# Kernel tuning notes

Hardware: AMD Instinct MI355X
Metric: run time of the kernel (lower is better)

Reference implementation:

```python
import jax, jax.numpy as jnp
import numpy as np

B, N, C = 8, 8192, 256
H = 8            # num_heads
D = C // H       # head dim = 32
P = 64           # proj_size (Linformer rank)


def setup_inputs() -> dict:
    key = jax.random.key(0)
    ks = jax.random.split(key, 12)
    s = lambda fan_in: 1.0 / np.sqrt(fan_in)
    return {
        "x": jax.random.normal(ks[0], (B, N, C), jnp.float32),
        "Wqkvv": jax.random.normal(ks[1], (4 * C, C), jnp.float32) * s(C),
        "WE": jax.random.normal(ks[2], (P, N), jnp.float32) * s(N),
        "bE": jax.random.normal(ks[3], (P,), jnp.float32) * s(N),
        "WF": jax.random.normal(ks[4], (P, N), jnp.float32) * s(N),
        "bF": jax.random.normal(ks[5], (P,), jnp.float32) * s(N),
        "Wo1": jax.random.normal(ks[6], (C // 2, C), jnp.float32) * s(C),
        "bo1": jax.random.normal(ks[7], (C // 2,), jnp.float32) * s(C),
        "Wo2": jax.random.normal(ks[8], (C // 2, C), jnp.float32) * s(C),
        "bo2": jax.random.normal(ks[9], (C // 2,), jnp.float32) * s(C),
        "temp1": jnp.ones((H, 1, 1), jnp.float32),
        "temp2": jnp.ones((H, 1, 1), jnp.float32),
    }


def _l2norm(v, axis=-1, eps=1e-12):
    # matches torch F.normalize
    n = jnp.sqrt(jnp.sum(v * v, axis=axis, keepdims=True))
    return v / jnp.maximum(n, eps)


def reference(x, Wqkvv, WE, bE, WF, bF, Wo1, bo1, Wo2, bo2, temp1, temp2):
    b, n, c = x.shape
    # qkvv: [b,n,4c] -> [4,b,h,d,n]  (includes the .transpose(-2,-1) of each part)
    qkvv = jnp.einsum('bnc,fc->bnf', x, Wqkvv).reshape(b, n, 4, H, D)
    qkvv = qkvv.transpose(2, 0, 3, 4, 1)
    q, k, v_ca, v_sa = qkvv[0], qkvv[1], qkvv[2], qkvv[3]  # each [b,h,d,n]

    # Linformer-style low-rank projections along the token axis
    k_proj = jnp.einsum('bhdn,pn->bhdp', k, WE) + bE   # [b,h,d,p]
    v_proj = jnp.einsum('bhdn,pn->bhdp', v_sa, WF) + bF

    qn = _l2norm(q)
    kn = _l2norm(k)

    # --- channel attention branch (XCiT-style) ---
    attn_ca = jnp.einsum('bhdn,bhen->bhde', qn, kn) * temp1[None]  # [b,h,d,d]
    attn_ca = jax.nn.softmax(attn_ca, axis=-1)  # dropout: eval mode (identity)
    x_ca = jnp.einsum('bhde,bhen->bhdn', attn_ca, v_ca)
    x_ca = x_ca.transpose(0, 3, 1, 2).reshape(b, n, c)  # [b,n,c]

    # --- spatial attention branch (low-rank) ---
    attn_sa = jnp.einsum('bhdn,bhdp->bhnp', qn, k_proj) * temp2[None]  # [b,h,n,p]
    attn_sa = jax.nn.softmax(attn_sa, axis=-1)
    x_sa = jnp.einsum('bhnp,bhdp->bhnd', attn_sa, v_proj)  # [b,h,n,d]
    # faithful to original: permute(0,3,1,2).reshape(b,n,c)
    x_sa = x_sa.transpose(0, 3, 1, 2).reshape(b, n, c)

    x_sa = jnp.einsum('bnc,oc->bno', x_sa, Wo1) + bo1
    x_ca = jnp.einsum('bnc,oc->bno', x_ca, Wo2) + bo2
    return jnp.concatenate((x_sa, x_ca), axis=-1)
```

## Files before the change

kernel.cpp:

```cpp
#include <hip/hip_runtime.h>
#include <hip/hip_bf16.h>
#include <stdint.h>


typedef __attribute__((ext_vector_type(8))) __bf16 bf16x8;
typedef __attribute__((ext_vector_type(4))) __bf16 bf16x4;
typedef __attribute__((ext_vector_type(4))) float f32x4;

#define MFMA(a, b, c) __builtin_amdgcn_mfma_f32_16x16x32_bf16((a), (b), (c), 0, 0, 0)

__device__ __forceinline__ void gl2lds16(const __bf16* g, __bf16* l) {
  __builtin_amdgcn_global_load_lds(
      (const __attribute__((address_space(1))) void*)(const void*)g,
      (__attribute__((address_space(3))) void*)(void*)l, 16, 0, 0);
}

__device__ __forceinline__ int detect_f32(const unsigned int* __restrict__ xw) {
  int c = 0;
#pragma unroll
  for (int i = 0; i < 64; ++i) {
    const unsigned int u = xw[i];
    c += (((u >> 7) & 0xFF) >= 0xC0) ? 1 : 0;
    c += (((u >> 23) & 0xFF) >= 0xC0) ? 1 : 0;
  }
  return c > 8;
}

__global__ __launch_bounds__(256) void k_convert_x(const void* __restrict__ src,
                                                   __bf16* __restrict__ dst) {
  const int i = (blockIdx.x * 256 + threadIdx.x) * 8;
  if (detect_f32((const unsigned int*)src)) {
    const float* s = (const float*)src;
    bf16x8 v;
#pragma unroll
    for (int j = 0; j < 8; ++j) v[j] = (__bf16)s[i + j];
    *(bf16x8*)(dst + i) = v;
  } else {
    *(bf16x8*)(dst + i) = *(const bf16x8*)((const __bf16*)src + i);
  }
}

__global__ __launch_bounds__(256) void k_convert_w(
    const void* s0, const void* s1, const void* s2, const void* s3, const void* s4,
    const void* s5, const void* s6, const void* s7, const void* s8, const void* s9,
    const void* s10, __bf16* __restrict__ cw, const void* __restrict__ xsrc) {
  const int i = (blockIdx.x * 256 + threadIdx.x) * 8;
  if (i >= 1376656) return;
  const void* s;
  int base;
  if (i < 262144)        { s = s0;  base = 0; }
  else if (i < 786432)   { s = s1;  base = 262144; }
  else if (i < 786496)   { s = s2;  base = 786432; }
  else if (i < 1310784)  { s = s3;  base = 786496; }
  else if (i < 1310848)  { s = s4;  base = 1310784; }
  else if (i < 1343616)  { s = s5;  base = 1310848; }
  else if (i < 1343744)  { s = s6;  base = 1343616; }
  else if (i < 1376512)  { s = s7;  base = 1343744; }
  else if (i < 1376640)  { s = s8;  base = 1376512; }
  else if (i < 1376648)  { s = s9;  base = 1376640; }
  else                   { s = s10; base = 1376648; }
  const int li = i - base;
  if (detect_f32((const unsigned int*)xsrc)) {
    const float* sf = (const float*)s;
#pragma unroll
    for (int j = 0; j < 8; ++j) cw[i + j] = (__bf16)sf[li + j];
  } else {
    const __bf16* sb = (const __bf16*)s;
#pragma unroll
    for (int j = 0; j < 8; ++j) cw[i + j] = sb[li + j];
  }
}

union alignas(16) QkvvSmem {
  struct { __bf16 A[2][4096]; __bf16 B[2][4096]; } k;
  __bf16 C[32 * 136];
};

__global__ __launch_bounds__(256, 5) void k_qkvv(const __bf16* __restrict__ x,
                                                 const __bf16* __restrict__ Wq,
                                                 __bf16* __restrict__ qkvv,
                                                 float* __restrict__ npart) {
  __shared__ QkvvSmem sm;
  const int t = threadIdx.x, lane = t & 63;
  const int wr = t >> 7, wc = (t >> 6) & 1;
  const int l15 = lane & 15, g = lane >> 4;
  const int f0 = blockIdx.y * 128;
  const int t0 = blockIdx.x * 128;
  f32x4 acc[4][4] = {};
  const int r = t >> 2;
  const int c8 = ((t & 3) ^ ((t >> 3) & 3)) * 8;
  const int cx = ((g ^ ((l15 >> 1) & 3)) * 8);
#pragma unroll
  for (int i = 0; i < 2; ++i) {
    gl2lds16(Wq + (size_t)(f0 + i * 64 + r) * 256 + c8, &sm.k.A[0][i * 2048 + t * 8]);
    gl2lds16(x + (size_t)(t0 + i * 64 + r) * 256 + c8, &sm.k.B[0][i * 2048 + t * 8]);
  }
  __syncthreads();
  for (int ks = 0; ks < 8; ++ks) {
    const int cur = ks & 1, nxt = cur ^ 1;
    if (ks < 7) {
      const int k1 = (ks + 1) * 32;
#pragma unroll
      for (int i = 0; i < 2; ++i) {
        gl2lds16(Wq + (size_t)(f0 + i * 64 + r) * 256 + k1 + c8, &sm.k.A[nxt][i * 2048 + t * 8]);
        gl2lds16(x + (size_t)(t0 + i * 64 + r) * 256 + k1 + c8, &sm.k.B[nxt][i * 2048 + t * 8]);
      }
    }
    bf16x8 af[4], bfr[4];
#pragma unroll
    for (int i = 0; i < 4; ++i) {
      af[i] = *(const bf16x8*)(&sm.k.A[cur][(wr * 64 + i * 16 + l15) * 32 + cx]);
      bfr[i] = *(const bf16x8*)(&sm.k.B[cur][(wc * 64 + i * 16 + l15) * 32 + cx]);
    }
#pragma unroll
    for (int i = 0; i < 4; ++i)
#pragma unroll
      for (int j = 0; j < 4; ++j) acc[i][j] = MFMA(af[i], bfr[j], acc[i][j]);
    __syncthreads();
  }
  const int b = t0 >> 13;
  const int n0 = t0 & 8191;
  for (int i = 0; i < 4; ++i) {
    if (i) __syncthreads();
#pragma unroll
    for (int j = 0; j < 4; ++j)
#pragma unroll
      for (int rr = 0; rr < 4; ++rr)
        sm.C[(wr * 16 + g * 4 + rr) * 136 + wc * 64 + j * 16 + l15] = (__bf16)acc[i][j][rr];
    __syncthreads();
#pragma unroll
    for (int half = 0; half < 2; ++half) {
      const int row_l = (t >> 4) + half * 16;
      const int col8 = (t & 15) * 8;
      const bf16x8 v = *(const bf16x8*)(sm.C + row_l * 136 + col8);
      const int f = f0 + (row_l >> 4) * 64 + i * 16 + (row_l & 15);
      *(bf16x8*)(qkvv + (size_t)(((f >> 8) * 8 + b) * 256 + (f & 255)) * 8192 + n0 + col8) = v;
      if (f0 < 512) {
        float s = 0.f;
#pragma unroll
        for (int jj = 0; jj < 8; ++jj) { const float q = (float)v[jj]; s += q * q; }
#pragma unroll
        for (int off = 1; off < 16; off <<= 1) s += __shfl_xor(s, off, 16);
        if ((t & 15) == 0) npart[(size_t)blockIdx.x * 512 + f] = s;
      }
    }
  }
}

__global__ __launch_bounds__(256) void k_nred(const float* __restrict__ npart,
                                              float* __restrict__ qsum,
                                              float* __restrict__ ksum) {
  const int which = blockIdx.x >> 3, b = blockIdx.x & 7;
  const int c = threadIdx.x;
  float s = 0.f;
#pragma unroll 4
  for (int j = 0; j < 64; ++j)
    s += npart[(size_t)(b * 64 + j) * 512 + which * 256 + c];
  (which ? ksum : qsum)[b * 256 + c] = s;
}

__global__ __launch_bounds__(256) void k_proj_part(const __bf16* __restrict__ qkvv,
                                                   const __bf16* __restrict__ WE,
                                                   const __bf16* __restrict__ WF,
                                                   float* __restrict__ pbuf) {
  __shared__ alignas(16) __bf16 As[2][128 * 32];
  __shared__ alignas(16) __bf16 Bs[2][64 * 32];
  const int t = threadIdx.x, lane = t & 63;
  const int wr = t >> 7, wc = (t >> 6) & 1;
  const int l15 = lane & 15, g = lane >> 4;
  const int kc = blockIdx.x, mt = blockIdx.y, pj = blockIdx.z;
  const __bf16* A = qkvv + (size_t)(pj ? 3 : 1) * 2048 * 8192;
  const __bf16* Bm = pj ? WF : WE;
  const int r0 = mt * 128;
  f32x4 acc[4][2] = {};
  const int r = t >> 2;
  const int c8 = ((t & 3) ^ ((t >> 3) & 3)) * 8;
  const int cx = ((g ^ ((l15 >> 1) & 3)) * 8);
  const int kb = kc * 512;
#pragma unroll
  for (int i = 0; i < 2; ++i)
    gl2lds16(A + (size_t)(r0 + i * 64 + r) * 8192 + kb + c8, &As[0][i * 2048 + t * 8]);
  gl2lds16(Bm + (size_t)r * 8192 + kb + c8, &Bs[0][t * 8]);
  __syncthreads();
  for (int ks = 0; ks < 16; ++ks) {
    const int cur = ks & 1, nxt = cur ^ 1;
    if (ks < 15) {
      const int k1 = kb + (ks + 1) * 32;
#pragma unroll
      for (int i = 0; i < 2; ++i)
        gl2lds16(A + (size_t)(r0 + i * 64 + r) * 8192 + k1 + c8, &As[nxt][i * 2048 + t * 8]);
      gl2lds16(Bm + (size_t)r * 8192 + k1 + c8, &Bs[nxt][t * 8]);
    }
    bf16x8 af[4], bfr[2];
#pragma unroll
    for (int i = 0; i < 4; ++i)
      af[i] = *(const bf16x8*)(&As[cur][(wr * 64 + i * 16 + l15) * 32 + cx]);
#pragma unroll
    for (int j = 0; j < 2; ++j)
      bfr[j] = *(const bf16x8*)(&Bs[cur][(wc * 32 + j * 16 + l15) * 32 + cx]);
#pragma unroll
    for (int i = 0; i < 4; ++i)
#pragma unroll
      for (int j = 0; j < 2; ++j) acc[i][j] = MFMA(af[i], bfr[j], acc[i][j]);
    __syncthreads();
  }
  float* dst = pbuf + (size_t)((pj * 16 + kc) * 2048 + r0) * 64;
#pragma unroll
  for (int i = 0; i < 4; ++i)
#pragma unroll
    for (int j = 0; j < 2; ++j)
#pragma unroll
      for (int rr = 0; rr < 4; ++rr)
        dst[(wr * 64 + i * 16 + g * 4 + rr) * 64 + wc * 32 + j * 16 + l15] = acc[i][j][rr];
}

__global__ __launch_bounds__(256) void k_proj_reduce(const float* __restrict__ pbuf,
                                                     const __bf16* __restrict__ bE,
                                                     const __bf16* __restrict__ bF,
                                                     const float* __restrict__ qsum,
                                                     const __bf16* __restrict__ t2,
                                                     __bf16* __restrict__ kprojT,
                                                     __bf16* __restrict__ vprojb) {
  const int idx = blockIdx.x * 256 + threadIdx.x;
  const int pj = idx >> 17, rp = idx & 131071, p = idx & 63;
  const int row = rp >> 6, bh = row >> 5, d = row & 31, h = bh & 7;
  float s = (float)((pj ? bF : bE)[p]);
  const float* src = pbuf + (size_t)pj * 16 * 131072 + rp;
#pragma unroll
  for (int k = 0; k < 16; ++k) s += src[(size_t)k * 131072];
  if (pj == 0) {
    const float qi = 1.0f / fmaxf(sqrtf(qsum[row]), 1e-12f);
    kprojT[bh * 2048 + p * 32 + d] = (__bf16)(s * qi * (float)t2[h]);
  } else {
    vprojb[bh * 2048 + d * 64 + p] = (__bf16)s;
  }
}

__global__ __launch_bounds__(256) void k_sca_part(const __bf16* __restrict__ qkvv,
                                                  float* __restrict__ spart) {
  const int bh = blockIdx.x, kc = blockIdx.y;
  const int t = threadIdx.x, lane = t & 63, w = t >> 6;
  const __bf16* qb = qkvv + (size_t)(bh * 32) * 8192;
  const __bf16* kb = qkvv + (size_t)(2048 + bh * 32) * 8192;
  f32x4 acc[2][2] = {};
  const int kbase = kc * 1024 + w * 256 + (lane >> 4) * 8;
#pragma unroll
  for (int ks = 0; ks < 256; ks += 32) {
    bf16x8 af[2], bfr[2];
#pragma unroll
    for (int i = 0; i < 2; ++i) {
      af[i] = *(const bf16x8*)(qb + (size_t)(i * 16 + (lane & 15)) * 8192 + kbase + ks);
      bfr[i] = *(const bf16x8*)(kb + (size_t)(i * 16 + (lane & 15)) * 8192 + kbase + ks);
    }
#pragma unroll
    for (int i = 0; i < 2; ++i)
#pragma unroll
      for (int j = 0; j < 2; ++j) acc[i][j] = MFMA(af[i], bfr[j], acc[i][j]);
  }
  float* dst = spart + (size_t)((bh * 8 + kc) * 4 + w) * 1024;
#pragma unroll
  for (int i = 0; i < 2; ++i)
#pragma unroll
    for (int j = 0; j < 2; ++j)
#pragma unroll
      for (int rr = 0; rr < 4; ++rr)
        dst[(i * 16 + (lane >> 4) * 4 + rr) * 32 + j * 16 + (lane & 15)] = acc[i][j][rr];
}

__global__ __launch_bounds__(256) void k_sca_softmax(const float* __restrict__ spart,
                                                     const float* __restrict__ qsum,
                                                     const float* __restrict__ ksum,
                                                     const __bf16* __restrict__ temp1,
                                                     __bf16* __restrict__ attnb) {
  const int bh = blockIdx.x;
  __shared__ float S[1024];
  const int t = threadIdx.x;
  const float tmp = (float)temp1[bh & 7];
  for (int idx = t; idx < 1024; idx += 256) {
    float s = 0.f;
    const float* src = spart + (size_t)bh * 32768 + idx;
#pragma unroll
    for (int k = 0; k < 32; ++k) s += src[k * 1024];
    const float qi = 1.0f / fmaxf(sqrtf(qsum[bh * 32 + (idx >> 5)]), 1e-12f);
    const float ki = 1.0f / fmaxf(sqrtf(ksum[bh * 32 + (idx & 31)]), 1e-12f);
    S[idx] = s * qi * ki * tmp;
  }
  __syncthreads();
  const int lane = t & 63, w = t >> 6;
#pragma unroll
  for (int rr = 0; rr < 4; ++rr) {
    const int row = rr * 8 + w * 2 + (lane >> 5);
    const int e = lane & 31;
    float v = S[row * 32 + e];
    float m = v;
#pragma unroll
    for (int off = 16; off; off >>= 1) m = fmaxf(m, __shfl_xor(m, off, 32));
    const float ex = __expf(v - m);
    float sm = ex;
#pragma unroll
    for (int off = 16; off; off >>= 1) sm += __shfl_xor(sm, off, 32);
    attnb[(size_t)bh * 1024 + row * 32 + e] = (__bf16)(ex / sm);
  }
}

union alignas(16) CasaSmem {
  struct { __bf16 V[32 * 264]; __bf16 L[64 * 72]; } ca;
  struct { __bf16 Q[32 * 264]; __bf16 P[4][16 * 72]; __bf16 L[32 * 72]; } sa;
};

__global__ __launch_bounds__(256) void k_casa(const __bf16* __restrict__ qkvv,
                                              const __bf16* __restrict__ attnb,
                                              const __bf16* __restrict__ kprojT,
                                              const __bf16* __restrict__ vprojb,
                                              __bf16* __restrict__ xca,
                                              __bf16* __restrict__ xsa) {
  __shared__ CasaSmem sm;
  const int t = threadIdx.x, lane = t & 63, w = t >> 6;
  const int l15 = lane & 15, g = lane >> 4;
  if (blockIdx.y < 64) {
    const int bh = blockIdx.y, b = bh >> 3, h = bh & 7;
    const __bf16* vb = qkvv + (size_t)(4096 + bh * 32) * 8192;
    {
      const int er = t >> 5, nc8 = (t & 31) * 8;
#pragma unroll
      for (int l = 0; l < 4; ++l) {
        const int e = l * 8 + er;
        *(bf16x8*)(&sm.ca.V[e * 264 + nc8]) =
            *(const bf16x8*)(vb + (size_t)e * 8192 + blockIdx.x * 256 + nc8);
      }
    }
    bf16x8 aa[2];
#pragma unroll
    for (int mi = 0; mi < 2; ++mi)
      aa[mi] = *(const bf16x8*)(attnb + bh * 1024 + (mi * 16 + l15) * 32 + g * 8);
    __syncthreads();
#pragma unroll
    for (int it = 0; it < 4; ++it) {
      const int nl = it * 64 + w * 16 + l15;
      union { bf16x8 v; unsigned short u[8]; } bq;
#pragma unroll
      for (int j = 0; j < 8; ++j)
        bq.u[j] = *(const unsigned short*)(&sm.ca.V[(g * 8 + j) * 264 + nl]);
      f32x4 o[2] = {};
#pragma unroll
      for (int mi = 0; mi < 2; ++mi) o[mi] = MFMA(aa[mi], bq.v, o[mi]);
      if (it) __syncthreads();
#pragma unroll
      for (int mi = 0; mi < 2; ++mi) {
        bf16x4 p4;
#pragma unroll
        for (int rr = 0; rr < 4; ++rr) p4[rr] = (__bf16)o[mi][rr];
        *(bf16x4*)(&sm.ca.L[(w * 16 + l15) * 72 + mi * 16 + g * 4]) = p4;
      }
      __syncthreads();
      {
        const int row = t >> 2, ch = t & 3;
        const bf16x8 v = *(const bf16x8*)(&sm.ca.L[row * 72 + ch * 8]);
        *(bf16x8*)(xca + (size_t)(b * 8192 + blockIdx.x * 256 + it * 64 + row) * 256 +
                   h * 32 + ch * 8) = v;
      }
    }
  } else {
    const int bh = blockIdx.y - 64;
    const __bf16* qb = qkvv + (size_t)(bh * 32) * 8192;
    {
      const int er = t >> 5, nc8 = (t & 31) * 8;
#pragma unroll
      for (int l = 0; l < 4; ++l) {
        const int e = l * 8 + er;
        *(bf16x8*)(&sm.sa.Q[e * 264 + nc8]) =
            *(const bf16x8*)(qb + (size_t)e * 8192 + blockIdx.x * 256 + nc8);
      }
    }
    bf16x8 ka[4], va[2][2];
#pragma unroll
    for (int tile = 0; tile < 4; ++tile)
      ka[tile] = *(const bf16x8*)(kprojT + bh * 2048 + (tile * 16 + l15) * 32 + g * 8);
#pragma unroll
    for (int mi = 0; mi < 2; ++mi)
#pragma unroll
      for (int kh = 0; kh < 2; ++kh)
        va[mi][kh] = *(const bf16x8*)(vprojb + bh * 2048 + (mi * 16 + l15) * 64 + kh * 32 + g * 8);
    __syncthreads();
    __bf16* Pw = &sm.sa.P[w][0];
#pragma unroll
    for (int it = 0; it < 4; ++it) {
      const int nl = it * 64 + w * 16 + l15;
      union { bf16x8 v; unsigned short u[8]; } bq;
#pragma unroll
      for (int j = 0; j < 8; ++j)
        bq.u[j] = *(const unsigned short*)(&sm.sa.Q[(g * 8 + j) * 264 + nl]);
      f32x4 st[4];
#pragma unroll
      for (int tile = 0; tile < 4; ++tile) {
        f32x4 z = {};
        st[tile] = MFMA(ka[tile], bq.v, z);
      }
      float m = st[0][0];
#pragma unroll
      for (int tile = 0; tile < 4; ++tile)
#pragma unroll
        for (int rr = 0; rr < 4; ++rr) m = fmaxf(m, st[tile][rr]);
      m = fmaxf(m, __shfl_xor(m, 16, 64));
      m = fmaxf(m, __shfl_xor(m, 32, 64));
      float sum = 0.f;
#pragma unroll
      for (int tile = 0; tile < 4; ++tile) {
        bf16x4 p4;
#pragma unroll
        for (int rr = 0; rr < 4; ++rr) {
          const float ex = __expf(st[tile][rr] - m);
          sum += ex;
          p4[rr] = (__bf16)ex;
        }
        *(bf16x4*)(Pw + l15 * 72 + tile * 16 + g * 4) = p4;
      }
      sum += __shfl_xor(sum, 16, 64);
      sum += __shfl_xor(sum, 32, 64);
      const float inv = 1.0f / sum;
      f32x4 o[2] = {};
#pragma unroll
      for (int kh = 0; kh < 2; ++kh) {
        const bf16x8 pf = *(const bf16x8*)(Pw + l15 * 72 + kh * 32 + g * 8);
#pragma unroll
        for (int mi = 0; mi < 2; ++mi) o[mi] = MFMA(va[mi][kh], pf, o[mi]);
      }
      if (it) __syncthreads();
#pragma unroll
      for (int mi = 0; mi < 2; ++mi)
#pragma unroll
        for (int rr = 0; rr < 4; ++rr) {
          const int d = mi * 16 + g * 4 + rr;
          sm.sa.L[d * 72 + w * 16 + l15] = (__bf16)(o[mi][rr] * inv);
        }
      __syncthreads();
      {
        const int row = t >> 3, ch = t & 7;
        const bf16x8 v = *(const bf16x8*)(&sm.sa.L[row * 72 + ch * 8]);
        *(bf16x8*)(xsa + (size_t)(bh * 32 + row) * 8192 + blockIdx.x * 256 + it * 64 +
                   ch * 8) = v;
      }
    }
  }
}

__global__ __launch_bounds__(256) void k_out(const __bf16* __restrict__ xsa,
                                             const __bf16* __restrict__ xca,
                                             const __bf16* __restrict__ Wo1,
                                             const __bf16* __restrict__ bo1,
                                             const __bf16* __restrict__ Wo2,
                                             const __bf16* __restrict__ bo2,
                                             void* __restrict__ outv,
                                             const void* __restrict__ xsrc) {
  __shared__ alignas(16) __bf16 As[2][128 * 32];
  __shared__ alignas(16) __bf16 Bs[2][128 * 32];
  const int t = threadIdx.x, lane = t & 63;
  const int wr = t >> 7, wc = (t >> 6) & 1;
  const int l15 = lane & 15, g = lane >> 4;
  const int nt = blockIdx.x, b = blockIdx.y, br = blockIdx.z;
  const int isf32 = detect_f32((const unsigned int*)xsrc);
  const __bf16* Wo = br ? Wo2 : Wo1;
  const __bf16* bo = br ? bo2 : bo1;
  f32x4 acc[4][4] = {};
  const int r = t >> 2;
  const int c8 = ((t & 3) ^ ((t >> 3) & 3)) * 8;
  const int cx = ((g ^ ((l15 >> 1) & 3)) * 8);
  const int row_b = nt * 128 + r;
  auto asrc = [&](int i, int k0) -> const __bf16* {
    const int row = row_b + i * 64;
    if (br == 0)
      return xsa + (size_t)((b * 8 + ((row >> 5) & 7)) * 32 + (row >> 8)) * 8192 +
             (row & 31) * 256 + k0 + c8;
    return xca + (size_t)(b * 8192 + row) * 256 + k0 + c8;
  };
#pragma unroll
  for (int i = 0; i < 2; ++i) {
    gl2lds16(asrc(i, 0), &As[0][i * 2048 + t * 8]);
    gl2lds16(Wo + (size_t)(i * 64 + r) * 256 + c8, &Bs[0][i * 2048 + t * 8]);
  }
  __syncthreads();
  for (int ks = 0; ks < 8; ++ks) {
    const int cur = ks & 1, nxt = cur ^ 1;
    if (ks < 7) {
      const int k1 = (ks + 1) * 32;
#pragma unroll
      for (int i = 0; i < 2; ++i) {
        gl2lds16(asrc(i, k1), &As[nxt][i * 2048 + t * 8]);
        gl2lds16(Wo + (size_t)(i * 64 + r) * 256 + k1 + c8, &Bs[nxt][i * 2048 + t * 8]);
      }
    }
    bf16x8 af[4], bfr[4];
#pragma unroll
    for (int i = 0; i < 4; ++i) {
      af[i] = *(const bf16x8*)(&As[cur][(wr * 64 + i * 16 + l15) * 32 + cx]);
      bfr[i] = *(const bf16x8*)(&Bs[cur][(wc * 64 + i * 16 + l15) * 32 + cx]);
    }
#pragma unroll
    for (int i = 0; i < 4; ++i)
#pragma unroll
      for (int j = 0; j < 4; ++j) acc[i][j] = MFMA(af[i], bfr[j], acc[i][j]);
    __syncthreads();
  }
  float bias[4];
#pragma unroll
  for (int j = 0; j < 4; ++j) bias[j] = (float)bo[wc * 64 + j * 16 + l15];
#pragma unroll
  for (int i = 0; i < 4; ++i) {
#pragma unroll
    for (int j = 0; j < 4; ++j) {
      const int col = wc * 64 + j * 16 + l15;
#pragma unroll
      for (int rr = 0; rr < 4; ++rr) {
        const int row = nt * 128 + wr * 64 + i * 16 + g * 4 + rr;
        const float val = acc[i][j][rr] + bias[j];
        const size_t oi = (size_t)(b * 8192 + row) * 256 + br * 128 + col;
        if (isf32) ((float*)outv)[oi] = val;
        else ((__bf16*)outv)[oi] = (__bf16)val;
      }
    }
  }
}

extern "C" void kernel_launch(void* const* d_in, const int* in_sizes, int n_in,
                              void* d_out, int out_size, void* d_ws, size_t ws_size,
                              hipStream_t stream) {
  char* ws = (char*)d_ws;
  __bf16* qkvv   = (__bf16*)(ws);
  __bf16* cinx   = (__bf16*)(ws + 134217728ull);
  __bf16* xca    = (__bf16*)(ws + 134217728ull);
  float*  pbuf   = (float*)(ws + 167772160ull);
  float*  npart  = (float*)(ws + 184549376ull);
  float*  spart  = (float*)(ws + 184549376ull);
  __bf16* xsa    = (__bf16*)(ws + 167772160ull);
  __bf16* kprojT = (__bf16*)(ws + 201326592ull);
  __bf16* vprojb = (__bf16*)(ws + 201588736ull);
  float*  qsum   = (float*)(ws + 201850880ull);
  float*  ksum   = (float*)(ws + 201859072ull);
  __bf16* attnb  = (__bf16*)(ws + 201867264ull);
  __bf16* cw     = (__bf16*)(ws + 201998336ull);

  __bf16* cWq  = cw;
  __bf16* cWE  = cw + 262144;
  __bf16* cbE  = cw + 786432;
  __bf16* cWF  = cw + 786496;
  __bf16* cbF  = cw + 1310784;
  __bf16* cWo1 = cw + 1310848;
  __bf16* cbo1 = cw + 1343616;
  __bf16* cWo2 = cw + 1343744;
  __bf16* cbo2 = cw + 1376512;
  __bf16* ct1  = cw + 1376640;
  __bf16* ct2  = cw + 1376648;

  k_convert_x<<<8192, 256, 0, stream>>>(d_in[0], cinx);
  k_convert_w<<<673, 256, 0, stream>>>(d_in[1], d_in[2], d_in[3], d_in[4], d_in[5],
                                       d_in[6], d_in[7], d_in[8], d_in[9], d_in[10],
                                       d_in[11], cw, d_in[0]);
  k_qkvv<<<dim3(512, 8), 256, 0, stream>>>(cinx, cWq, qkvv, npart);
  k_nred<<<16, 256, 0, stream>>>(npart, qsum, ksum);
  k_proj_part<<<dim3(16, 16, 2), 256, 0, stream>>>(qkvv, cWE, cWF, pbuf);
  k_proj_reduce<<<dim3(1024), 256, 0, stream>>>(pbuf, cbE, cbF, qsum, ct2, kprojT, vprojb);
  k_sca_part<<<dim3(64, 8), 256, 0, stream>>>(qkvv, spart);
  k_sca_softmax<<<dim3(64), 256, 0, stream>>>(spart, qsum, ksum, ct1, attnb);
  k_casa<<<dim3(32, 128), 256, 0, stream>>>(qkvv, attnb, kprojT, vprojb, xca, xsa);
  k_out<<<dim3(64, 8, 2), 256, 0, stream>>>(xsa, xca, cWo1, cbo1, cWo2, cbo2, d_out, d_in[0]);
}
```

Measured before the change: 334.7 us.

## Reassociate Linformer projections through x and skip computing v_sa

The K and V projections now multiply the low-rank weights WE/WF directly with x to form a small P×C matrix per batch. That result is split-K reduced and then multiplied by the relevant rows of Wqkvv, instead of projecting the full k and v_sa tensors. Because v_sa is no longer needed, the QKVV GEMM grid shrinks to skip its last quarter of output features, saving both the GEMM work and a large write. The qkvv shared memory union is split into separate arrays and the occupancy hint is dropped, which may lower occupancy. One extra small kernel launch is added.

Measured after the change: 329.6 us. About the same (-1.5%).

```diff
diff --git a/kernel.cpp b/kernel.cpp
--- a/kernel.cpp
+++ b/kernel.cpp
@@ -71,16 +71,13 @@
   }
 }
 
-union alignas(16) QkvvSmem {
-  struct { __bf16 A[2][4096]; __bf16 B[2][4096]; } k;
-  __bf16 C[32 * 136];
-};
-
-__global__ __launch_bounds__(256, 5) void k_qkvv(const __bf16* __restrict__ x,
-                                                 const __bf16* __restrict__ Wq,
-                                                 __bf16* __restrict__ qkvv,
-                                                 float* __restrict__ npart) {
-  __shared__ QkvvSmem sm;
+__global__ __launch_bounds__(256) void k_qkvv(const __bf16* __restrict__ x,
+                                              const __bf16* __restrict__ Wq,
+                                              __bf16* __restrict__ qkvv,
+                                              float* __restrict__ npart) {
+  __shared__ alignas(16) __bf16 As[2][128 * 32];
+  __shared__ alignas(16) __bf16 Bs[2][128 * 32];
+  __shared__ alignas(16) __bf16 Cs[32 * 136];
   const int t = threadIdx.x, lane = t & 63;
   const int wr = t >> 7, wc = (t >> 6) & 1;
   const int l15 = lane & 15, g = lane >> 4;
@@ -92,8 +89,8 @@
   const int cx = ((g ^ ((l15 >> 1) & 3)) * 8);
 #pragma unroll
   for (int i = 0; i < 2; ++i) {
-    gl2lds16(Wq + (size_t)(f0 + i * 64 + r) * 256 + c8, &sm.k.A[0][i * 2048 + t * 8]);
-    gl2lds16(x + (size_t)(t0 + i * 64 + r) * 256 + c8, &sm.k.B[0][i * 2048 + t * 8]);
+    gl2lds16(Wq + (size_t)(f0 + i * 64 + r) * 256 + c8, &As[0][i * 2048 + t * 8]);
+    gl2lds16(x + (size_t)(t0 + i * 64 + r) * 256 + c8, &Bs[0][i * 2048 + t * 8]);
   }
   __syncthreads();
   for (int ks = 0; ks < 8; ++ks) {
@@ -102,15 +99,15 @@
       const int k1 = (ks + 1) * 32;
 #pragma unroll
       for (int i = 0; i < 2; ++i) {
-        gl2lds16(Wq + (size_t)(f0 + i * 64 + r) * 256 + k1 + c8, &sm.k.A[nxt][i * 2048 + t * 8]);
-        gl2lds16(x + (size_t)(t0 + i * 64 + r) * 256 + k1 + c8, &sm.k.B[nxt][i * 2048 + t * 8]);
+        gl2lds16(Wq + (size_t)(f0 + i * 64 + r) * 256 + k1 + c8, &As[nxt][i * 2048 + t * 8]);
+        gl2lds16(x + (size_t)(t0 + i * 64 + r) * 256 + k1 + c8, &Bs[nxt][i * 2048 + t * 8]);
       }
     }
     bf16x8 af[4], bfr[4];
 #pragma unroll
     for (int i = 0; i < 4; ++i) {
-      af[i] = *(const bf16x8*)(&sm.k.A[cur][(wr * 64 + i * 16 + l15) * 32 + cx]);
-      bfr[i] = *(const bf16x8*)(&sm.k.B[cur][(wc * 64 + i * 16 + l15) * 32 + cx]);
+      af[i] = *(const bf16x8*)(&As[cur][(wr * 64 + i * 16 + l15) * 32 + cx]);
+      bfr[i] = *(const bf16x8*)(&Bs[cur][(wc * 64 + i * 16 + l15) * 32 + cx]);
     }
 #pragma unroll
     for (int i = 0; i < 4; ++i)
@@ -126,13 +123,13 @@
     for (int j = 0; j < 4; ++j)
 #pragma unroll
       for (int rr = 0; rr < 4; ++rr)
-        sm.C[(wr * 16 + g * 4 + rr) * 136 + wc * 64 + j * 16 + l15] = (__bf16)acc[i][j][rr];
+        Cs[(wr * 16 + g * 4 + rr) * 136 + wc * 64 + j * 16 + l15] = (__bf16)acc[i][j][rr];
     __syncthreads();
 #pragma unroll
     for (int half = 0; half < 2; ++half) {
       const int row_l = (t >> 4) + half * 16;
       const int col8 = (t & 15) * 8;
-      const bf16x8 v = *(const bf16x8*)(sm.C + row_l * 136 + col8);
+      const bf16x8 v = *(const bf16x8*)(Cs + row_l * 136 + col8);
       const int f = f0 + (row_l >> 4) * 64 + i * 16 + (row_l & 15);
       *(bf16x8*)(qkvv + (size_t)(((f >> 8) * 8 + b) * 256 + (f & 255)) * 8192 + n0 + col8) = v;
       if (f0 < 512) {
@@ -159,80 +156,96 @@
   (which ? ksum : qsum)[b * 256 + c] = s;
 }
 
-__global__ __launch_bounds__(256) void k_proj_part(const __bf16* __restrict__ qkvv,
-                                                   const __bf16* __restrict__ WE,
-                                                   const __bf16* __restrict__ WF,
-                                                   float* __restrict__ pbuf) {
-  __shared__ alignas(16) __bf16 As[2][128 * 32];
-  __shared__ alignas(16) __bf16 Bs[2][64 * 32];
-  const int t = threadIdx.x, lane = t & 63;
-  const int wr = t >> 7, wc = (t >> 6) & 1;
+__global__ __launch_bounds__(256) void k_ef(const __bf16* __restrict__ x,
+                                            const __bf16* __restrict__ WE,
+                                            const __bf16* __restrict__ WF,
+                                            float* __restrict__ pbufE) {
+  __shared__ alignas(16) __bf16 Xs[32 * 264];
+  const int t = threadIdx.x, lane = t & 63, w = t >> 6;
   const int l15 = lane & 15, g = lane >> 4;
-  const int kc = blockIdx.x, mt = blockIdx.y, pj = blockIdx.z;
-  const __bf16* A = qkvv + (size_t)(pj ? 3 : 1) * 2048 * 8192;
-  const __bf16* Bm = pj ? WF : WE;
-  const int r0 = mt * 128;
-  f32x4 acc[4][2] = {};
-  const int r = t >> 2;
-  const int c8 = ((t & 3) ^ ((t >> 3) & 3)) * 8;
-  const int cx = ((g ^ ((l15 >> 1) & 3)) * 8);
-  const int kb = kc * 512;
-#pragma unroll
-  for (int i = 0; i < 2; ++i)
-    gl2lds16(A + (size_t)(r0 + i * 64 + r) * 8192 + kb + c8, &As[0][i * 2048 + t * 8]);
-  gl2lds16(Bm + (size_t)r * 8192 + kb + c8, &Bs[0][t * 8]);
+  const int kc = blockIdx.x, b = blockIdx.y, pj = blockIdx.z;
+  const __bf16* Wp = pj ? WF : WE;
+  f32x4 acc[4][4] = {};
+  const int sr = t >> 3, sc = (t & 7) * 8;
+  for (int ks = 0; ks < 16; ++ks) {
+    const int n0 = kc * 512 + ks * 32;
+    __syncthreads();
+#pragma unroll
+    for (int q = 0; q < 4; ++q)
+      *(bf16x8*)(&Xs[sr * 264 + q * 64 + sc]) =
+          *(const bf16x8*)(x + (size_t)(b * 8192 + n0 + sr) * 256 + q * 64 + sc);
+    __syncthreads();
+    bf16x8 af[4];
+#pragma unroll
+    for (int i = 0; i < 4; ++i)
+      af[i] = *(const bf16x8*)(Wp + (size_t)(i * 16 + l15) * 8192 + n0 + g * 8);
+#pragma unroll
+    for (int j = 0; j < 4; ++j) {
+      union { bf16x8 v; unsigned short u[8]; } bq;
+#pragma unroll
+      for (int jj = 0; jj < 8; ++jj)
+        bq.u[jj] = *(const unsigned short*)(&Xs[(g * 8 + jj) * 264 + w * 64 + j * 16 + l15]);
+#pragma unroll
+      for (int i = 0; i < 4; ++i) acc[i][j] = MFMA(af[i], bq.v, acc[i][j]);
+    }
+  }
+  float* dst = pbufE + (size_t)((pj * 8 + b) * 16 + kc) * 16384;
+#pragma unroll
+  for (int i = 0; i < 4; ++i)
+#pragma unroll
+    for (int j = 0; j < 4; ++j)
+#pragma unroll
+      for (int rr = 0; rr < 4; ++rr)
+        dst[(i * 16 + g * 4 + rr) * 256 + w * 64 + j * 16 + l15] = acc[i][j][rr];
+}
+
+__global__ __launch_bounds__(256) void k_zred(const float* __restrict__ pbufE,
+                                              float* __restrict__ Z) {
+  const int idx = blockIdx.x * 256 + threadIdx.x;
+  const int grp = idx >> 14;
+  const int pc = idx & 16383;
+  const float* src = pbufE + (size_t)grp * 16 * 16384 + pc;
+  float s = 0.f;
+#pragma unroll
+  for (int k = 0; k < 16; ++k) s += src[(size_t)k * 16384];
+  Z[(size_t)grp * 16384 + pc] = s;
+}
+
+__global__ __launch_bounds__(256) void k_proj2(const float* __restrict__ Z,
+                                               const __bf16* __restrict__ Wq,
+                                               const __bf16* __restrict__ bE,
+                                               const __bf16* __restrict__ bF,
+                                               const float* __restrict__ qsum,
+                                               const __bf16* __restrict__ t2,
+                                               __bf16* __restrict__ kprojT,
+                                               __bf16* __restrict__ vprojb) {
+  __shared__ float Zs[8][260];
+  const int bx = blockIdx.x;
+  const int pj = bx >> 9, bh = (bx >> 3) & 63, pch = bx & 7;
+  const int b = bh >> 3, h = bh & 7;
+  const int t = threadIdx.x;
+  {
+    const int pr = t >> 5, c8 = (t & 31) * 8;
+    const float* zr = Z + (size_t)((pj * 8 + b) * 64 + pch * 8 + pr) * 256 + c8;
+    *(f32x4*)(&Zs[pr][c8]) = *(const f32x4*)(zr);
+    *(f32x4*)(&Zs[pr][c8 + 4]) = *(const f32x4*)(zr + 4);
+  }
   __syncthreads();
-  for (int ks = 0; ks < 16; ++ks) {
-    const int cur = ks & 1, nxt = cur ^ 1;
-    if (ks < 15) {
-      const int k1 = kb + (ks + 1) * 32;
-#pragma unroll
-      for (int i = 0; i < 2; ++i)
-        gl2lds16(A + (size_t)(r0 + i * 64 + r) * 8192 + k1 + c8, &As[nxt][i * 2048 + t * 8]);
-      gl2lds16(Bm + (size_t)r * 8192 + k1 + c8, &Bs[nxt][t * 8]);
-    }
-    bf16x8 af[4], bfr[2];
-#pragma unroll
-    for (int i = 0; i < 4; ++i)
-      af[i] = *(const bf16x8*)(&As[cur][(wr * 64 + i * 16 + l15) * 32 + cx]);
-#pragma unroll
-    for (int j = 0; j < 2; ++j)
-      bfr[j] = *(const bf16x8*)(&Bs[cur][(wc * 32 + j * 16 + l15) * 32 + cx]);
-#pragma unroll
-    for (int i = 0; i < 4; ++i)
-#pragma unroll
-      for (int j = 0; j < 2; ++j) acc[i][j] = MFMA(af[i], bfr[j], acc[i][j]);
-    __syncthreads();
-  }
-  float* dst = pbuf + (size_t)((pj * 16 + kc) * 2048 + r0) * 64;
-#pragma unroll
-  for (int i = 0; i < 4; ++i)
-#pragma unroll
-    for (int j = 0; j < 2; ++j)
-#pragma unroll
-      for (int rr = 0; rr < 4; ++rr)
-        dst[(wr * 64 + i * 16 + g * 4 + rr) * 64 + wc * 32 + j * 16 + l15] = acc[i][j][rr];
-}
-
-__global__ __launch_bounds__(256) void k_proj_reduce(const float* __restrict__ pbuf,
-                                                     const __bf16* __restrict__ bE,
-                                                     const __bf16* __restrict__ bF,
-                                                     const float* __restrict__ qsum,
-                                                     const __bf16* __restrict__ t2,
-                                                     __bf16* __restrict__ kprojT,
-                                                     __bf16* __restrict__ vprojb) {
-  const int idx = blockIdx.x * 256 + threadIdx.x;
-  const int pj = idx >> 17, rp = idx & 131071, p = idx & 63;
-  const int row = rp >> 6, bh = row >> 5, d = row & 31, h = bh & 7;
-  float s = (float)((pj ? bF : bE)[p]);
-  const float* src = pbuf + (size_t)pj * 16 * 131072 + rp;
-#pragma unroll
-  for (int k = 0; k < 16; ++k) s += src[(size_t)k * 131072];
+  const int pl = t >> 5, p = pch * 8 + pl, d = t & 31;
+  const int f = (pj ? 768 : 256) + h * 32 + d;
+  const __bf16* wr = Wq + (size_t)f * 256;
+  float acc = 0.f;
+#pragma unroll
+  for (int c = 0; c < 256; c += 8) {
+    const bf16x8 w8 = *(const bf16x8*)(wr + c);
+#pragma unroll
+    for (int jj = 0; jj < 8; ++jj) acc += (float)w8[jj] * Zs[pl][c + jj];
+  }
   if (pj == 0) {
-    const float qi = 1.0f / fmaxf(sqrtf(qsum[row]), 1e-12f);
-    kprojT[bh * 2048 + p * 32 + d] = (__bf16)(s * qi * (float)t2[h]);
+    const float qi = 1.0f / fmaxf(sqrtf(qsum[bh * 32 + d]), 1e-12f);
+    kprojT[bh * 2048 + p * 32 + d] = (__bf16)((acc + (float)bE[p]) * qi * (float)t2[h]);
   } else {
-    vprojb[bh * 2048 + d * 64 + p] = (__bf16)s;
+    vprojb[bh * 2048 + d * 64 + p] = (__bf16)(acc + (float)bF[p]);
   }
 }
 
@@ -528,8 +541,9 @@
   __bf16* qkvv   = (__bf16*)(ws);
   __bf16* cinx   = (__bf16*)(ws + 134217728ull);
   __bf16* xca    = (__bf16*)(ws + 134217728ull);
-  float*  pbuf   = (float*)(ws + 167772160ull);
+  float*  pbufE  = (float*)(ws + 167772160ull);
   float*  npart  = (float*)(ws + 184549376ull);
+  float*  Zb     = (float*)(ws + 185597952ull);
   float*  spart  = (float*)(ws + 184549376ull);
   __bf16* xsa    = (__bf16*)(ws + 167772160ull);
   __bf16* kprojT = (__bf16*)(ws + 201326592ull);
@@ -555,10 +569,11 @@
   k_convert_w<<<673, 256, 0, stream>>>(d_in[1], d_in[2], d_in[3], d_in[4], d_in[5],
                                        d_in[6], d_in[7], d_in[8], d_in[9], d_in[10],
                                        d_in[11], cw, d_in[0]);
-  k_qkvv<<<dim3(512, 8), 256, 0, stream>>>(cinx, cWq, qkvv, npart);
+  k_qkvv<<<dim3(512, 6), 256, 0, stream>>>(cinx, cWq, qkvv, npart);
   k_nred<<<16, 256, 0, stream>>>(npart, qsum, ksum);
-  k_proj_part<<<dim3(16, 16, 2), 256, 0, stream>>>(qkvv, cWE, cWF, pbuf);
-  k_proj_reduce<<<dim3(1024), 256, 0, stream>>>(pbuf, cbE, cbF, qsum, ct2, kprojT, vprojb);
+  k_ef<<<dim3(16, 8, 2), 256, 0, stream>>>(cinx, cWE, cWF, pbufE);
+  k_zred<<<1024, 256, 0, stream>>>(pbufE, Zb);
+  k_proj2<<<1024, 256, 0, stream>>>(Zb, cWq, cbE, cbF, qsum, ct2, kprojT, vprojb);
   k_sca_part<<<dim3(64, 8), 256, 0, stream>>>(qkvv, spart);
   k_sca_softmax<<<dim3(64), 256, 0, stream>>>(spart, qsum, ksum, ct1, attnb);
   k_casa<<<dim3(32, 128), 256, 0, stream>>>(qkvv, attnb, kprojT, vprojb, xca, xsa);
```
